# Kernel tuning notes

Measured on AMD Instinct MI355X. Metric: run time of the kernel, lower is better.

Reference implementation:

```python
import jax, jax.numpy as jnp
import numpy as np

N = 300000   # number of edges
MUL = 64     # multiplicity of each input irrep block
MID = 2 * MUL  # 128, simplified mid multiplicity per l


def setup_inputs() -> dict:
    key = jax.random.key(0)
    ks = jax.random.split(key, 12)
    inp = {
        # x: irreps 64x0e+64x1o -> [N, 64 + 64*3]
        "x": jax.random.normal(ks[0], (N, MUL + MUL * 3), dtype=jnp.float32),
        # y: irreps 1x0e+1x1o -> [N, 4] (edge spherical harmonics)
        "y": jax.random.normal(ks[1], (N, 4), dtype=jnp.float32),
        # scalars: 64x0e radial embedding
        "scalars": jax.random.normal(ks[2], (N, 64), dtype=jnp.float32),
        # uvw tensor-product weights, one [MUL, MUL] matrix per path (v dim = 1 squeezed)
        "W_tp1": jax.random.normal(ks[3], (MUL, MUL), dtype=jnp.float32),  # 0e x 0e -> 0e
        "W_tp2": jax.random.normal(ks[4], (MUL, MUL), dtype=jnp.float32),  # 0e x 1o -> 1o
        "W_tp3": jax.random.normal(ks[5], (MUL, MUL), dtype=jnp.float32),  # 1o x 0e -> 1o
        "W_tp4": jax.random.normal(ks[6], (MUL, MUL), dtype=jnp.float32),  # 1o x 1o -> 0e
        # radial MLP [64, 64, 64, 256]
        "W_fc1": jax.random.normal(ks[7], (64, 64), dtype=jnp.float32),
        "W_fc2": jax.random.normal(ks[8], (64, 64), dtype=jnp.float32),
        "W_fc3": jax.random.normal(ks[9], (64, 2 * MID), dtype=jnp.float32),
        # equivariant linear mix per l: 128 -> 64
        "W_lin0": jax.random.normal(ks[10], (MID, MUL), dtype=jnp.float32),
        "W_lin1": jax.random.normal(ks[11], (MID, MUL), dtype=jnp.float32),
    }
    return inp


def reference(x, y, scalars, W_tp1, W_tp2, W_tp3, W_tp4,
              W_fc1, W_fc2, W_fc3, W_lin0, W_lin1):
    n = x.shape[0]
    x0 = x[:, :MUL]                          # [N, 64]   0e
    x1 = x[:, MUL:].reshape(n, MUL, 3)       # [N, 64, 3] 1o
    y0 = y[:, 0:1]                           # [N, 1]    0e
    y1 = y[:, 1:4]                           # [N, 3]    1o

    inv_sqrt_mul = 1.0 / jnp.sqrt(jnp.float32(MUL))   # path normalization (fan_in = mul1*mul2)
    inv_sqrt3 = 1.0 / jnp.sqrt(jnp.float32(3.0))      # CG coeff for 1o x 1o -> 0e

    # --- uvw tensor product (4 paths), irreps_mid = 128x0e + 128x1o ---
    mid0a = ((x0 * y0) @ W_tp1) * inv_sqrt_mul                                 # [N,128? no: N,64] 0e
    mid0b = ((jnp.einsum('num,nm->nu', x1, y1) * inv_sqrt3) @ W_tp4) * inv_sqrt_mul  # [N,64] 0e
    mid1a = (x0 @ W_tp2)[:, :, None] * y1[:, None, :] * inv_sqrt_mul           # [N,64,3] 1o
    mid1b = jnp.einsum('num,uw->nwm', x1 * y0[:, :, None], W_tp3) * inv_sqrt_mul  # [N,64,3] 1o

    mid0 = jnp.concatenate([mid0a, mid0b], axis=1)   # [N,128]
    mid1 = jnp.concatenate([mid1a, mid1b], axis=1)   # [N,128,3]

    # --- radial MLP generating per-edge uvu scaling weights ---
    inv8 = 1.0 / jnp.sqrt(jnp.float32(64))
    h = jax.nn.silu((scalars @ W_fc1) * inv8)
    h = jax.nn.silu((h @ W_fc2) * inv8)
    w = (h @ W_fc3) * inv8                           # [N, 256]
    w0, w1 = w[:, :MID], w[:, MID:]

    # --- uvu scaling (tp of mid with 1x0e ones, per-edge weights) ---
    s0 = mid0 * w0                                   # [N,128]
    s1 = mid1 * w1[:, :, None]                       # [N,128,3]

    # --- o3.Linear 128x0e+128x1o -> 64x0e+64x1o ---
    inv_sqrt_mid = 1.0 / jnp.sqrt(jnp.float32(MID))
    out0 = (s0 @ W_lin0) * inv_sqrt_mid              # [N,64]
    out1 = jnp.einsum('num,uw->nwm', s1, W_lin1) * inv_sqrt_mid  # [N,64,3]

    return jnp.concatenate([out0, out1.reshape(n, MUL * 3)], axis=1)  # [N,256]
```

## Files before the change

### kernel.cpp

```cpp
#include <hip/hip_runtime.h>

typedef _Float16 f16x8 __attribute__((ext_vector_type(8)));
typedef float    f32x4 __attribute__((ext_vector_type(4)));

#define NROWS  300000
#define NTILES (NROWS/16)
#define WPB    8
#define TPB    512
#define NBLK   ((NTILES + WPB - 1) / WPB)

#define LSCALE     2048.0f
#define INV_LSCALE 4.8828125e-4f

#define RS64   136
#define LO64   72
#define RS128  264
#define LO128  136

#define IMG_P1 0
#define IMG_P2 17408
#define IMG_P3 34816
#define IMG_P4 52224
#define IMG_P5 78336
#define IMG_P6 95232
#define IMG_TOT 120832

#define BUFSZ  26112
#define OFF_A  0
#define OFF_B  BUFSZ
#define OFF_SBUF (2*BUFSZ)
#define SB_WAVE 1280
#define LDS_HALVES (OFF_SBUF + WPB*SB_WAVE)
static_assert(LDS_HALVES * 2 <= 160*1024, "LDS overflow");

struct fp16p { f16x8 h, l; };
struct h2 { _Float16 h, l; };
struct acc2 { f32x4 m, l; };

__device__ __forceinline__ f32x4 MFMA(f16x8 a, f16x8 b, f32x4 c) {
  return __builtin_amdgcn_mfma_f32_16x16x32_f16(a, b, c, 0, 0, 0);
}

__device__ __forceinline__ void gemm2(const fp16p& A0, const fp16p& B0,
                                      const fp16p& A1, const fp16p& B1, acc2& c) {
  c.m = MFMA(A0.h, B0.h, c.m);
  c.m = MFMA(A0.l, B0.h, c.m);
  c.l = MFMA(A0.h, B0.l, c.l);
  c.m = MFMA(A1.h, B1.h, c.m);
  c.m = MFMA(A1.l, B1.h, c.m);
  c.l = MFMA(A1.h, B1.l, c.l);
}
__device__ __forceinline__ f32x4 fin(const acc2& c) { return c.m + c.l * INV_LSCALE; }

__device__ __forceinline__ fp16p bfragp(const _Float16* w, int RS, int LO,
                                        int nt, int ks, int lane) {
  const _Float16* base = w + (nt*16 + (lane & 15))*RS + ks*32 + (lane >> 4)*8;
  fp16p r;
  r.h = *(const f16x8*)base;
  r.l = *(const f16x8*)(base + LO);
  return r;
}

__device__ __forceinline__ h2 split1(float v) {
  h2 r;
  r.h = (_Float16)v;
  r.l = (_Float16)(v - (float)r.h);
  return r;
}

__device__ __forceinline__ fp16p split8(const float* p, float s) {
  f32x4 a = *(const f32x4*)p, b = *(const f32x4*)(p + 4);
  fp16p r;
#pragma unroll
  for (int i = 0; i < 4; ++i) {
    h2 t0 = split1(a[i]*s);
    h2 t1 = split1(b[i]*s);
    r.h[i]   = t0.h; r.l[i]   = t0.l;
    r.h[4+i] = t1.h; r.l[4+i] = t1.l;
  }
  return r;
}

__device__ __forceinline__ void load24(const float* p, float* vv) {
#pragma unroll
  for (int i = 0; i < 6; ++i) {
    f32x4 t = *(const f32x4*)(p + 4*i);
    vv[4*i+0] = t[0]; vv[4*i+1] = t[1]; vv[4*i+2] = t[2]; vv[4*i+3] = t[3];
  }
}

__device__ __forceinline__ void copyimg(_Float16* ldsdst, const _Float16* gsrc,
                                        int nch, int wave, int lane) {
  for (int c = wave; c < nch; c += WPB)
    __builtin_amdgcn_global_load_lds(
        (const __attribute__((address_space(1))) void*)(gsrc + c*512 + lane*8),
        (__attribute__((address_space(3))) void*)(ldsdst + c*512), 16, 0, 0);
}

#define LGKM0() asm volatile("s_waitcnt lgkmcnt(0)" ::: "memory")

__global__ __launch_bounds__(256) void prep_w(
    const float* __restrict__ Wtp1, const float* __restrict__ Wtp2,
    const float* __restrict__ Wtp3, const float* __restrict__ Wtp4,
    const float* __restrict__ Wfc1, const float* __restrict__ Wfc2,
    const float* __restrict__ Wfc3, const float* __restrict__ Wlin0,
    const float* __restrict__ Wlin1, _Float16* __restrict__ ws)
{
  int e = blockIdx.x*256 + threadIdx.x;
  const float INV8 = 0.125f, INVS3 = 0.57735026918962576f, INVSMD = 0.08838834764831845f;
  const float* W; int u, n; _Float16* dst; int RS, LOo; float sc;
  if (e < 4096)       { int l = e;        u=l>>6; n=l&63;  W=Wfc1 +u*64+n;  dst=ws+IMG_P1;       RS=RS64;  LOo=LO64;  sc=INV8; }
  else if (e < 8192)  { int l = e-4096;   u=l>>6; n=l&63;  W=Wfc2 +u*64+n;  dst=ws+IMG_P1+8704;  RS=RS64;  LOo=LO64;  sc=INV8; }
  else if (e < 24576) { int l = e-8192;   u=l>>8; n=l&255; W=Wfc3 +u*256+n; RS=RS64; LOo=LO64; sc=INV8;
                        if (n < 128) dst = ws+IMG_P2; else { dst = ws+IMG_P3; n -= 128; } }
  else if (e < 28672) { int l = e-24576;  u=l>>6; n=l&63;  W=Wtp1 +u*64+n;  dst=ws+IMG_P4;       RS=RS64;  LOo=LO64;  sc=INV8; }
  else if (e < 32768) { int l = e-28672;  u=l>>6; n=l&63;  W=Wtp2 +u*64+n;  dst=ws+IMG_P4+8704;  RS=RS64;  LOo=LO64;  sc=INV8; }
  else if (e < 36864) { int l = e-32768;  u=l>>6; n=l&63;  W=Wtp4 +u*64+n;  dst=ws+IMG_P4+17408; RS=RS64;  LOo=LO64;  sc=INV8*INVS3; }
  else if (e < 45056) { int l = e-36864;  u=l>>6; n=l&63;  W=Wlin0+u*64+n;  dst=ws+IMG_P5;       RS=RS128; LOo=LO128; sc=INVSMD; }
  else if (e < 49152) { int l = e-45056;  u=l>>6; n=l&63;  W=Wtp3 +u*64+n;  dst=ws+IMG_P6;       RS=RS64;  LOo=LO64;  sc=INV8; }
  else                { int l = e-49152;  u=l>>6; n=l&63;  W=Wlin1+u*64+n;  dst=ws+IMG_P6+8704;  RS=RS128; LOo=LO128; sc=INVSMD; }
  float v = (*W) * sc;
  _Float16 h = (_Float16)v;
  float res = (v - (float)h) * LSCALE;
  dst[n*RS + u]       = h;
  dst[n*RS + LOo + u] = (_Float16)res;
}

__global__ __launch_bounds__(TPB, 2) void tp_fused(
    const float* __restrict__ x,    const float* __restrict__ y,
    const float* __restrict__ sc,
    const _Float16* __restrict__ wsrc, float* __restrict__ out)
{
  __shared__ _Float16 lds[LDS_HALVES];
  const int tid = threadIdx.x;
  const int lane = tid & 63;
  const int wave = tid >> 6;
  const int tile = blockIdx.x * WPB + wave;
  const bool active = (tile < NTILES);
  const int r0   = (active ? tile : 0) * 16;
  const int arow = lane & 15;
  const int kgrp = lane >> 4;
  const int rowg = r0 + arow;
  _Float16* bufA = lds + OFF_A;
  _Float16* bufB = lds + OFF_B;
  _Float16* swbh = lds + OFF_SBUF + wave*SB_WAVE;
  _Float16* swbl = swbh + 640;

  copyimg(bufA, wsrc + IMG_P1, 34, wave, lane);

  const float yv = y[r0*4 + lane];
  const float y0A  = __shfl(yv, arow*4 + 0);
  const float y1A0 = __shfl(yv, arow*4 + 1);
  const float y1A1 = __shfl(yv, arow*4 + 2);
  const float y1A2 = __shfl(yv, arow*4 + 3);
  float y1D[3][4];
#pragma unroll
  for (int m = 0; m < 3; ++m)
#pragma unroll
    for (int r = 0; r < 4; ++r)
      y1D[m][r] = __shfl(yv, (kgrp*4 + r)*4 + 1 + m);

  const int rbase = ((arow & 3)*4 + (arow >> 2))*40;
  auto bounce = [&](const f32x4* zz, bool do_silu, fp16p& A0, fp16p& A1) {
#pragma unroll
    for (int c = 0; c < 2; ++c) {
      LGKM0();
#pragma unroll
      for (int ntl = 0; ntl < 2; ++ntl)
#pragma unroll
        for (int r = 0; r < 4; ++r) {
          float v = zz[c*2 + ntl][r];
          if (do_silu) v = v / (1.f + __expf(-v));
          h2 t = split1(v);
          int o = (r*4 + kgrp)*40 + ntl*16 + arow;
          swbh[o] = t.h;
          swbl[o] = t.l;
        }
      LGKM0();
      fp16p& A = c ? A1 : A0;
      A.h = *(const f16x8*)(swbh + rbase + kgrp*8);
      A.l = *(const f16x8*)(swbl + rbase + kgrp*8);
    }
  };

  const float* scp = sc + rowg*64;
  fp16p A0 = split8(scp + kgrp*8, 1.f);
  fp16p A1 = split8(scp + 32 + kgrp*8, 1.f);

  __syncthreads();
  copyimg(bufB, wsrc + IMG_P2, 34, wave, lane);

  f32x4 z[4];
#pragma unroll
  for (int nt = 0; nt < 4; ++nt) {
    acc2 c{};
    gemm2(A0, bfragp(bufA, RS64, LO64, nt, 0, lane),
          A1, bfragp(bufA, RS64, LO64, nt, 1, lane), c);
    z[nt] = fin(c);
  }
  bounce(z, true, A0, A1);

  f32x4 z2[4];
#pragma unroll
  for (int nt = 0; nt < 4; ++nt) {
    acc2 c{};
    gemm2(A0, bfragp(bufA + 8704, RS64, LO64, nt, 0, lane),
          A1, bfragp(bufA + 8704, RS64, LO64, nt, 1, lane), c);
    z2[nt] = fin(c);
  }
  bounce(z2, true, A0, A1);

  __syncthreads();
  copyimg(bufA, wsrc + IMG_P3, 34, wave, lane);

  f32x4 w[16];
#pragma unroll
  for (int nt = 0; nt < 8; ++nt) {
    acc2 c{};
    gemm2(A0, bfragp(bufB, RS64, LO64, nt, 0, lane),
          A1, bfragp(bufB, RS64, LO64, nt, 1, lane), c);
    w[nt] = fin(c);
  }

  __syncthreads();
  copyimg(bufB, wsrc + IMG_P4, 51, wave, lane);

#pragma unroll
  for (int nt = 0; nt < 8; ++nt) {
    acc2 c{};
    gemm2(A0, bfragp(bufA, RS64, LO64, nt, 0, lane),
          A1, bfragp(bufA, RS64, LO64, nt, 1, lane), c);
    w[8 + nt] = fin(c);
  }

  __syncthreads();
  copyimg(bufA, wsrc + IMG_P5, 33, wave, lane);

  const float* xr = x + rowg*256;
  fp16p X0 = split8(xr + kgrp*8, 1.f);
  fp16p X1 = split8(xr + 32 + kgrp*8, 1.f);
  fp16p Aa0 = split8(xr + kgrp*8, y0A);
  fp16p Aa1 = split8(xr + 32 + kgrp*8, y0A);

  f32x4 t4[4];
  f32x4 m0[8];
#pragma unroll
  for (int nt = 0; nt < 4; ++nt) {
    acc2 ct{}, cm{};
    gemm2(X0,  bfragp(bufB + 8704, RS64, LO64, nt, 0, lane),
          X1,  bfragp(bufB + 8704, RS64, LO64, nt, 1, lane), ct);
    gemm2(Aa0, bfragp(bufB, RS64, LO64, nt, 0, lane),
          Aa1, bfragp(bufB, RS64, LO64, nt, 1, lane), cm);
    t4[nt] = fin(ct);
    m0[nt] = fin(cm);
  }

  fp16p B40, B41;
  {
    float vv[24];
    load24(xr + 64 + 3*(kgrp*8), vv);
#pragma unroll
    for (int j = 0; j < 8; ++j) {
      h2 t = split1(vv[3*j]*y1A0 + vv[3*j+1]*y1A1 + vv[3*j+2]*y1A2);
      B40.h[j] = t.h; B40.l[j] = t.l;
    }
    load24(xr + 64 + 3*(32 + kgrp*8), vv);
#pragma unroll
    for (int j = 0; j < 8; ++j) {
      h2 t = split1(vv[3*j]*y1A0 + vv[3*j+1]*y1A1 + vv[3*j+2]*y1A2);
      B41.h[j] = t.h; B41.l[j] = t.l;
    }
  }
#pragma unroll
  for (int nt = 0; nt < 4; ++nt) {
    acc2 c{};
    gemm2(B40, bfragp(bufB + 17408, RS64, LO64, nt, 0, lane),
          B41, bfragp(bufB + 17408, RS64, LO64, nt, 1, lane), c);
    m0[4+nt] = fin(c);
  }

  __syncthreads();
  copyimg(bufB, wsrc + IMG_P6, 50, wave, lane);

  acc2 o0c[4] = {};
#pragma unroll
  for (int half = 0; half < 2; ++half) {
    f32x4 s[4];
#pragma unroll
    for (int nt = 0; nt < 4; ++nt)
#pragma unroll
      for (int r = 0; r < 4; ++r)
        s[nt][r] = m0[half*4 + nt][r] * w[half*4 + nt][r];
    fp16p S0, S1;
    bounce(s, false, S0, S1);
#pragma unroll
    for (int nt = 0; nt < 4; ++nt)
      gemm2(S0, bfragp(bufA, RS128, LO128, nt, half*2+0, lane),
            S1, bfragp(bufA, RS128, LO128, nt, half*2+1, lane), o0c[nt]);
  }
  if (active) {
#pragma unroll
    for (int nt = 0; nt < 4; ++nt) {
      f32x4 v = fin(o0c[nt]);
#pragma unroll
      for (int r = 0; r < 4; ++r)
        out[(r0 + kgrp*4 + r)*256 + nt*16 + arow] = v[r];
    }
  }

  __syncthreads();

  f32x4 o1f[3][4];
#pragma unroll
  for (int m = 0; m < 3; ++m) {
    fp16p C0, C1;
    {
      float vv[24];
      load24(xr + 64 + 3*(kgrp*8), vv);
#pragma unroll
      for (int j = 0; j < 8; ++j) {
        h2 t = split1(vv[3*j + m] * y0A);
        C0.h[j] = t.h; C0.l[j] = t.l;
      }
      load24(xr + 64 + 3*(32 + kgrp*8), vv);
#pragma unroll
      for (int j = 0; j < 8; ++j) {
        h2 t = split1(vv[3*j + m] * y0A);
        C1.h[j] = t.h; C1.l[j] = t.l;
      }
    }
    f32x4 mb[4];
#pragma unroll
    for (int nt = 0; nt < 4; ++nt) {
      acc2 c{};
      gemm2(C0, bfragp(bufB, RS64, LO64, nt, 0, lane),
            C1, bfragp(bufB, RS64, LO64, nt, 1, lane), c);
      mb[nt] = fin(c);
    }

    acc2 o1c[4] = {};
    {
      f32x4 s[4];
#pragma unroll
      for (int nt = 0; nt < 4; ++nt)
#pragma unroll
        for (int r = 0; r < 4; ++r)
          s[nt][r] = t4[nt][r] * y1D[m][r] * w[8 + nt][r];
      fp16p S0, S1;
      bounce(s, false, S0, S1);
#pragma unroll
      for (int nt = 0; nt < 4; ++nt)
        gemm2(S0, bfragp(bufB + 8704, RS128, LO128, nt, 0, lane),
              S1, bfragp(bufB + 8704, RS128, LO128, nt, 1, lane), o1c[nt]);
    }
    {
      f32x4 s[4];
#pragma unroll
      for (int nt = 0; nt < 4; ++nt)
#pragma unroll
        for (int r = 0; r < 4; ++r)
          s[nt][r] = mb[nt][r] * w[12 + nt][r];
      fp16p S0, S1;
      bounce(s, false, S0, S1);
#pragma unroll
      for (int nt = 0; nt < 4; ++nt)
        gemm2(S0, bfragp(bufB + 8704, RS128, LO128, nt, 2, lane),
              S1, bfragp(bufB + 8704, RS128, LO128, nt, 3, lane), o1c[nt]);
    }
#pragma unroll
    for (int nt = 0; nt < 4; ++nt)
      o1f[m][nt] = fin(o1c[nt]);
  }

  if (active) {
#pragma unroll
    for (int nt = 0; nt < 4; ++nt)
#pragma unroll
      for (int r = 0; r < 4; ++r) {
        float* p = out + (r0 + kgrp*4 + r)*256 + 64 + (nt*16 + arow)*3;
        p[0] = o1f[0][nt][r];
        p[1] = o1f[1][nt][r];
        p[2] = o1f[2][nt][r];
      }
  }
}

extern "C" void kernel_launch(void* const* d_in, const int* in_sizes, int n_in,
                              void* d_out, int out_size, void* d_ws, size_t ws_size,
                              hipStream_t stream) {
  (void)in_sizes; (void)n_in; (void)out_size; (void)ws_size;
  _Float16* ws = (_Float16*)d_ws;
  prep_w<<<224, 256, 0, stream>>>(
      (const float*)d_in[3],  (const float*)d_in[4],  (const float*)d_in[5],
      (const float*)d_in[6],  (const float*)d_in[7],  (const float*)d_in[8],
      (const float*)d_in[9],  (const float*)d_in[10], (const float*)d_in[11], ws);
  tp_fused<<<NBLK, TPB, 0, stream>>>(
      (const float*)d_in[0],  (const float*)d_in[1],  (const float*)d_in[2],
      ws, (float*)d_out);
}
```

Measured before the change: 328.1 us.

## Use transposed 16x16x16 MFMA formulation to drop LDS bounce between layers

Reformulates every GEMM so weights act as the A operand and activations as the B operand, using the 16x16x16 f16 MFMA. In this form each layer's accumulator layout matches the next layer's input fragment layout, so the per-wave LDS bounce buffer, the shuffles and the lgkmcnt waits can be removed, and output rows are written as contiguous float4 stores. The trade-off is twice as many, smaller MFMA instructions and more LDS weight fragment loads of half width, with more registers held for the activation fragments.

```diff
diff --git a/kernel.cpp b/kernel.cpp
--- a/kernel.cpp
+++ b/kernel.cpp
@@ -1,6 +1,6 @@
 #include <hip/hip_runtime.h>
 
-typedef _Float16 f16x8 __attribute__((ext_vector_type(8)));
+typedef _Float16 f16x4 __attribute__((ext_vector_type(4)));
 typedef float    f32x4 __attribute__((ext_vector_type(4)));
 
 #define NROWS  300000
@@ -23,41 +23,35 @@
 #define IMG_P4 52224
 #define IMG_P5 78336
 #define IMG_P6 95232
-#define IMG_TOT 120832
 
 #define BUFSZ  26112
 #define OFF_A  0
 #define OFF_B  BUFSZ
-#define OFF_SBUF (2*BUFSZ)
-#define SB_WAVE 1280
-#define LDS_HALVES (OFF_SBUF + WPB*SB_WAVE)
+#define LDS_HALVES (2*BUFSZ)
 static_assert(LDS_HALVES * 2 <= 160*1024, "LDS overflow");
 
-struct fp16p { f16x8 h, l; };
-struct h2 { _Float16 h, l; };
-struct acc2 { f32x4 m, l; };
-
-__device__ __forceinline__ f32x4 MFMA(f16x8 a, f16x8 b, f32x4 c) {
-  return __builtin_amdgcn_mfma_f32_16x16x32_f16(a, b, c, 0, 0, 0);
-}
-
-__device__ __forceinline__ void gemm2(const fp16p& A0, const fp16p& B0,
-                                      const fp16p& A1, const fp16p& B1, acc2& c) {
-  c.m = MFMA(A0.h, B0.h, c.m);
-  c.m = MFMA(A0.l, B0.h, c.m);
-  c.l = MFMA(A0.h, B0.l, c.l);
-  c.m = MFMA(A1.h, B1.h, c.m);
-  c.m = MFMA(A1.l, B1.h, c.m);
-  c.l = MFMA(A1.h, B1.l, c.l);
+struct apair { f16x4 h, l; };
+struct bpair { f16x4 h, l; };
+struct h2    { _Float16 h, l; };
+struct acc2  { f32x4 m, l; };
+
+__device__ __forceinline__ f32x4 MFMA16(f16x4 a, f16x4 b, f32x4 c) {
+  return __builtin_amdgcn_mfma_f32_16x16x16f16(a, b, c, 0, 0, 0);
+}
+
+__device__ __forceinline__ void gemmT(const apair& a, const bpair& b, acc2& c) {
+  c.m = MFMA16(a.h, b.h, c.m);
+  c.m = MFMA16(a.h, b.l, c.m);
+  c.l = MFMA16(a.l, b.h, c.l);
 }
 __device__ __forceinline__ f32x4 fin(const acc2& c) { return c.m + c.l * INV_LSCALE; }
 
-__device__ __forceinline__ fp16p bfragp(const _Float16* w, int RS, int LO,
-                                        int nt, int ks, int lane) {
-  const _Float16* base = w + (nt*16 + (lane & 15))*RS + ks*32 + (lane >> 4)*8;
-  fp16p r;
-  r.h = *(const f16x8*)base;
-  r.l = *(const f16x8*)(base + LO);
+__device__ __forceinline__ apair afrag(const _Float16* w, int RS, int LO,
+                                       int nt, int ks, int lane) {
+  const _Float16* base = w + (nt*16 + (lane & 15))*RS + ks*16 + ((lane >> 4) << 2);
+  apair r;
+  r.h = *(const f16x4*)base;
+  r.l = *(const f16x4*)(base + LO);
   return r;
 }
 
@@ -68,25 +62,14 @@
   return r;
 }
 
-__device__ __forceinline__ fp16p split8(const float* p, float s) {
-  f32x4 a = *(const f32x4*)p, b = *(const f32x4*)(p + 4);
-  fp16p r;
+__device__ __forceinline__ bpair splitB(f32x4 v) {
+  bpair r;
 #pragma unroll
   for (int i = 0; i < 4; ++i) {
-    h2 t0 = split1(a[i]*s);
-    h2 t1 = split1(b[i]*s);
-    r.h[i]   = t0.h; r.l[i]   = t0.l;
-    r.h[4+i] = t1.h; r.l[4+i] = t1.l;
+    h2 t = split1(v[i]);
+    r.h[i] = t.h; r.l[i] = t.l;
   }
   return r;
-}
-
-__device__ __forceinline__ void load24(const float* p, float* vv) {
-#pragma unroll
-  for (int i = 0; i < 6; ++i) {
-    f32x4 t = *(const f32x4*)(p + 4*i);
-    vv[4*i+0] = t[0]; vv[4*i+1] = t[1]; vv[4*i+2] = t[2]; vv[4*i+3] = t[3];
-  }
 }
 
 __device__ __forceinline__ void copyimg(_Float16* ldsdst, const _Float16* gsrc,
@@ -96,8 +79,6 @@
         (const __attribute__((address_space(1))) void*)(gsrc + c*512 + lane*8),
         (__attribute__((address_space(3))) void*)(ldsdst + c*512), 16, 0, 0);
 }
-
-#define LGKM0() asm volatile("s_waitcnt lgkmcnt(0)" ::: "memory")
 
 __global__ __launch_bounds__(256) void prep_w(
     const float* __restrict__ Wtp1, const float* __restrict__ Wtp2,
@@ -132,7 +113,7 @@
     const _Float16* __restrict__ wsrc, float* __restrict__ out)
 {
   __shared__ _Float16 lds[LDS_HALVES];
-  const int tid = threadIdx.x;
+  const int tid  = threadIdx.x;
   const int lane = tid & 63;
   const int wave = tid >> 6;
   const int tile = blockIdx.x * WPB + wave;
@@ -143,241 +124,188 @@
   const int rowg = r0 + arow;
   _Float16* bufA = lds + OFF_A;
   _Float16* bufB = lds + OFF_B;
-  _Float16* swbh = lds + OFF_SBUF + wave*SB_WAVE;
-  _Float16* swbl = swbh + 640;
 
   copyimg(bufA, wsrc + IMG_P1, 34, wave, lane);
 
-  const float yv = y[r0*4 + lane];
-  const float y0A  = __shfl(yv, arow*4 + 0);
-  const float y1A0 = __shfl(yv, arow*4 + 1);
-  const float y1A1 = __shfl(yv, arow*4 + 2);
-  const float y1A2 = __shfl(yv, arow*4 + 3);
-  float y1D[3][4];
-#pragma unroll
-  for (int m = 0; m < 3; ++m)
-#pragma unroll
-    for (int r = 0; r < 4; ++r)
-      y1D[m][r] = __shfl(yv, (kgrp*4 + r)*4 + 1 + m);
-
-  const int rbase = ((arow & 3)*4 + (arow >> 2))*40;
-  auto bounce = [&](const f32x4* zz, bool do_silu, fp16p& A0, fp16p& A1) {
-#pragma unroll
-    for (int c = 0; c < 2; ++c) {
-      LGKM0();
-#pragma unroll
-      for (int ntl = 0; ntl < 2; ++ntl)
-#pragma unroll
-        for (int r = 0; r < 4; ++r) {
-          float v = zz[c*2 + ntl][r];
-          if (do_silu) v = v / (1.f + __expf(-v));
-          h2 t = split1(v);
-          int o = (r*4 + kgrp)*40 + ntl*16 + arow;
-          swbh[o] = t.h;
-          swbl[o] = t.l;
-        }
-      LGKM0();
-      fp16p& A = c ? A1 : A0;
-      A.h = *(const f16x8*)(swbh + rbase + kgrp*8);
-      A.l = *(const f16x8*)(swbl + rbase + kgrp*8);
+  f32x4 yr = *(const f32x4*)(y + rowg*4);
+  const float y0A = yr[0], y1A0 = yr[1], y1A1 = yr[2], y1A2 = yr[3];
+
+  const float* scp = sc + rowg*64;
+  bpair SC[4];
+#pragma unroll
+  for (int ks = 0; ks < 4; ++ks)
+    SC[ks] = splitB(*(const f32x4*)(scp + ks*16 + kgrp*4));
+
+  __syncthreads();
+  copyimg(bufB, wsrc + IMG_P2, 34, wave, lane);
+
+  bpair H[4];
+#pragma unroll
+  for (int nt = 0; nt < 4; ++nt) {
+    acc2 c{};
+#pragma unroll
+    for (int ks = 0; ks < 4; ++ks)
+      gemmT(afrag(bufA, RS64, LO64, nt, ks, lane), SC[ks], c);
+    f32x4 v = fin(c);
+#pragma unroll
+    for (int i = 0; i < 4; ++i) v[i] = v[i] / (1.f + __expf(-v[i]));
+    H[nt] = splitB(v);
+  }
+  bpair H2[4];
+#pragma unroll
+  for (int nt = 0; nt < 4; ++nt) {
+    acc2 c{};
+#pragma unroll
+    for (int ks = 0; ks < 4; ++ks)
+      gemmT(afrag(bufA + 8704, RS64, LO64, nt, ks, lane), H[ks], c);
+    f32x4 v = fin(c);
+#pragma unroll
+    for (int i = 0; i < 4; ++i) v[i] = v[i] / (1.f + __expf(-v[i]));
+    H2[nt] = splitB(v);
+  }
+
+  __syncthreads();
+  copyimg(bufA, wsrc + IMG_P3, 34, wave, lane);
+
+  f32x4 wv[16];
+#pragma unroll
+  for (int nt = 0; nt < 8; ++nt) {
+    acc2 c{};
+#pragma unroll
+    for (int ks = 0; ks < 4; ++ks)
+      gemmT(afrag(bufB, RS64, LO64, nt, ks, lane), H2[ks], c);
+    wv[nt] = fin(c);
+  }
+
+  __syncthreads();
+  copyimg(bufB, wsrc + IMG_P4, 51, wave, lane);
+
+#pragma unroll
+  for (int nt = 0; nt < 8; ++nt) {
+    acc2 c{};
+#pragma unroll
+    for (int ks = 0; ks < 4; ++ks)
+      gemmT(afrag(bufA, RS64, LO64, nt, ks, lane), H2[ks], c);
+    wv[8 + nt] = fin(c);
+  }
+
+  __syncthreads();
+  copyimg(bufA, wsrc + IMG_P5, 33, wave, lane);
+
+  const float* xr = x + rowg*256;
+  bpair X[4], Xa[4];
+#pragma unroll
+  for (int ks = 0; ks < 4; ++ks) {
+    f32x4 v = *(const f32x4*)(xr + ks*16 + kgrp*4);
+    X[ks]  = splitB(v);
+    Xa[ks] = splitB(v * y0A);
+  }
+
+  f32x4 t4T[4], m0T[8];
+#pragma unroll
+  for (int nt = 0; nt < 4; ++nt) {
+    acc2 ct{}, cm{};
+#pragma unroll
+    for (int ks = 0; ks < 4; ++ks) {
+      gemmT(afrag(bufB + 8704, RS64, LO64, nt, ks, lane), X[ks],  ct);
+      gemmT(afrag(bufB,        RS64, LO64, nt, ks, lane), Xa[ks], cm);
     }
-  };
-
-  const float* scp = sc + rowg*64;
-  fp16p A0 = split8(scp + kgrp*8, 1.f);
-  fp16p A1 = split8(scp + 32 + kgrp*8, 1.f);
-
-  __syncthreads();
-  copyimg(bufB, wsrc + IMG_P2, 34, wave, lane);
-
-  f32x4 z[4];
-#pragma unroll
-  for (int nt = 0; nt < 4; ++nt) {
-    acc2 c{};
-    gemm2(A0, bfragp(bufA, RS64, LO64, nt, 0, lane),
-          A1, bfragp(bufA, RS64, LO64, nt, 1, lane), c);
-    z[nt] = fin(c);
-  }
-  bounce(z, true, A0, A1);
-
-  f32x4 z2[4];
-#pragma unroll
-  for (int nt = 0; nt < 4; ++nt) {
-    acc2 c{};
-    gemm2(A0, bfragp(bufA + 8704, RS64, LO64, nt, 0, lane),
-          A1, bfragp(bufA + 8704, RS64, LO64, nt, 1, lane), c);
-    z2[nt] = fin(c);
-  }
-  bounce(z2, true, A0, A1);
-
-  __syncthreads();
-  copyimg(bufA, wsrc + IMG_P3, 34, wave, lane);
-
-  f32x4 w[16];
-#pragma unroll
-  for (int nt = 0; nt < 8; ++nt) {
-    acc2 c{};
-    gemm2(A0, bfragp(bufB, RS64, LO64, nt, 0, lane),
-          A1, bfragp(bufB, RS64, LO64, nt, 1, lane), c);
-    w[nt] = fin(c);
-  }
-
-  __syncthreads();
-  copyimg(bufB, wsrc + IMG_P4, 51, wave, lane);
-
-#pragma unroll
-  for (int nt = 0; nt < 8; ++nt) {
-    acc2 c{};
-    gemm2(A0, bfragp(bufA, RS64, LO64, nt, 0, lane),
-          A1, bfragp(bufA, RS64, LO64, nt, 1, lane), c);
-    w[8 + nt] = fin(c);
-  }
-
-  __syncthreads();
-  copyimg(bufA, wsrc + IMG_P5, 33, wave, lane);
-
-  const float* xr = x + rowg*256;
-  fp16p X0 = split8(xr + kgrp*8, 1.f);
-  fp16p X1 = split8(xr + 32 + kgrp*8, 1.f);
-  fp16p Aa0 = split8(xr + kgrp*8, y0A);
-  fp16p Aa1 = split8(xr + 32 + kgrp*8, y0A);
-
-  f32x4 t4[4];
-  f32x4 m0[8];
-#pragma unroll
-  for (int nt = 0; nt < 4; ++nt) {
-    acc2 ct{}, cm{};
-    gemm2(X0,  bfragp(bufB + 8704, RS64, LO64, nt, 0, lane),
-          X1,  bfragp(bufB + 8704, RS64, LO64, nt, 1, lane), ct);
-    gemm2(Aa0, bfragp(bufB, RS64, LO64, nt, 0, lane),
-          Aa1, bfragp(bufB, RS64, LO64, nt, 1, lane), cm);
-    t4[nt] = fin(ct);
-    m0[nt] = fin(cm);
-  }
-
-  fp16p B40, B41;
-  {
-    float vv[24];
-    load24(xr + 64 + 3*(kgrp*8), vv);
-#pragma unroll
-    for (int j = 0; j < 8; ++j) {
-      h2 t = split1(vv[3*j]*y1A0 + vv[3*j+1]*y1A1 + vv[3*j+2]*y1A2);
-      B40.h[j] = t.h; B40.l[j] = t.l;
+    t4T[nt] = fin(ct);
+    m0T[nt] = fin(cm);
+  }
+
+  bpair A1[4];
+#pragma unroll
+  for (int ks = 0; ks < 4; ++ks) {
+    const float* p = xr + 64 + (16*ks + 4*kgrp)*3;
+    f32x4 q0 = *(const f32x4*)p, q1 = *(const f32x4*)(p+4), q2 = *(const f32x4*)(p+8);
+    float vv[12];
+#pragma unroll
+    for (int i = 0; i < 4; ++i) { vv[i] = q0[i]; vv[4+i] = q1[i]; vv[8+i] = q2[i]; }
+    f32x4 a;
+#pragma unroll
+    for (int e = 0; e < 4; ++e)
+      a[e] = vv[3*e]*y1A0 + vv[3*e+1]*y1A1 + vv[3*e+2]*y1A2;
+    A1[ks] = splitB(a);
+  }
+#pragma unroll
+  for (int nt = 0; nt < 4; ++nt) {
+    acc2 c{};
+#pragma unroll
+    for (int ks = 0; ks < 4; ++ks)
+      gemmT(afrag(bufB + 17408, RS64, LO64, nt, ks, lane), A1[ks], c);
+    m0T[4 + nt] = fin(c);
+  }
+
+  __syncthreads();
+  copyimg(bufB, wsrc + IMG_P6, 50, wave, lane);
+
+  bpair S[8];
+#pragma unroll
+  for (int ks = 0; ks < 8; ++ks)
+    S[ks] = splitB(m0T[ks] * wv[ks]);
+#pragma unroll
+  for (int nt = 0; nt < 4; ++nt) {
+    acc2 c{};
+#pragma unroll
+    for (int ks = 0; ks < 8; ++ks)
+      gemmT(afrag(bufA, RS128, LO128, nt, ks, lane), S[ks], c);
+    if (active)
+      *(f32x4*)(out + (size_t)rowg*256 + nt*16 + kgrp*4) = fin(c);
+  }
+
+  __syncthreads();
+
+  f32x4 o1f[3][4];
+#pragma unroll
+  for (int m = 0; m < 3; ++m) {
+    const float y1m = (m == 0) ? y1A0 : (m == 1) ? y1A1 : y1A2;
+    bpair C[4];
+#pragma unroll
+    for (int ks = 0; ks < 4; ++ks) {
+      const float* p = xr + 64 + (16*ks + 4*kgrp)*3;
+      f32x4 q0 = *(const f32x4*)p, q1 = *(const f32x4*)(p+4), q2 = *(const f32x4*)(p+8);
+      float vv[12];
+#pragma unroll
+      for (int i = 0; i < 4; ++i) { vv[i] = q0[i]; vv[4+i] = q1[i]; vv[8+i] = q2[i]; }
+      f32x4 a;
+#pragma unroll
+      for (int e = 0; e < 4; ++e) a[e] = vv[3*e + m] * y0A;
+      C[ks] = splitB(a);
     }
-    load24(xr + 64 + 3*(32 + kgrp*8), vv);
-#pragma unroll
-    for (int j = 0; j < 8; ++j) {
-      h2 t = split1(vv[3*j]*y1A0 + vv[3*j+1]*y1A1 + vv[3*j+2]*y1A2);
-      B41.h[j] = t.h; B41.l[j] = t.l;
-    }
-  }
-#pragma unroll
-  for (int nt = 0; nt < 4; ++nt) {
-    acc2 c{};
-    gemm2(B40, bfragp(bufB + 17408, RS64, LO64, nt, 0, lane),
-          B41, bfragp(bufB + 17408, RS64, LO64, nt, 1, lane), c);
-    m0[4+nt] = fin(c);
-  }
-
-  __syncthreads();
-  copyimg(bufB, wsrc + IMG_P6, 50, wave, lane);
-
-  acc2 o0c[4] = {};
-#pragma unroll
-  for (int half = 0; half < 2; ++half) {
-    f32x4 s[4];
-#pragma unroll
-    for (int nt = 0; nt < 4; ++nt)
-#pragma unroll
-      for (int r = 0; r < 4; ++r)
-        s[nt][r] = m0[half*4 + nt][r] * w[half*4 + nt][r];
-    fp16p S0, S1;
-    bounce(s, false, S0, S1);
-#pragma unroll
-    for (int nt = 0; nt < 4; ++nt)
-      gemm2(S0, bfragp(bufA, RS128, LO128, nt, half*2+0, lane),
-            S1, bfragp(bufA, RS128, LO128, nt, half*2+1, lane), o0c[nt]);
-  }
-  if (active) {
-#pragma unroll
-    for (int nt = 0; nt < 4; ++nt) {
-      f32x4 v = fin(o0c[nt]);
-#pragma unroll
-      for (int r = 0; r < 4; ++r)
-        out[(r0 + kgrp*4 + r)*256 + nt*16 + arow] = v[r];
-    }
-  }
-
-  __syncthreads();
-
-  f32x4 o1f[3][4];
-#pragma unroll
-  for (int m = 0; m < 3; ++m) {
-    fp16p C0, C1;
-    {
-      float vv[24];
-      load24(xr + 64 + 3*(kgrp*8), vv);
-#pragma unroll
-      for (int j = 0; j < 8; ++j) {
-        h2 t = split1(vv[3*j + m] * y0A);
-        C0.h[j] = t.h; C0.l[j] = t.l;
-      }
-      load24(xr + 64 + 3*(32 + kgrp*8), vv);
-#pragma unroll
-      for (int j = 0; j < 8; ++j) {
-        h2 t = split1(vv[3*j + m] * y0A);
-        C1.h[j] = t.h; C1.l[j] = t.l;
-      }
-    }
-    f32x4 mb[4];
+    f32x4 mbT[4];
 #pragma unroll
     for (int nt = 0; nt < 4; ++nt) {
       acc2 c{};
-      gemm2(C0, bfragp(bufB, RS64, LO64, nt, 0, lane),
-            C1, bfragp(bufB, RS64, LO64, nt, 1, lane), c);
-      mb[nt] = fin(c);
+#pragma unroll
+      for (int ks = 0; ks < 4; ++ks)
+        gemmT(afrag(bufB, RS64, LO64, nt, ks, lane), C[ks], c);
+      mbT[nt] = fin(c);
     }
 
-    acc2 o1c[4] = {};
-    {
-      f32x4 s[4];
-#pragma unroll
-      for (int nt = 0; nt < 4; ++nt)
-#pragma unroll
-        for (int r = 0; r < 4; ++r)
-          s[nt][r] = t4[nt][r] * y1D[m][r] * w[8 + nt][r];
-      fp16p S0, S1;
-      bounce(s, false, S0, S1);
-#pragma unroll
-      for (int nt = 0; nt < 4; ++nt)
-        gemm2(S0, bfragp(bufB + 8704, RS128, LO128, nt, 0, lane),
-              S1, bfragp(bufB + 8704, RS128, LO128, nt, 1, lane), o1c[nt]);
+    bpair S1[8];
+#pragma unroll
+    for (int ks = 0; ks < 4; ++ks)
+      S1[ks] = splitB(t4T[ks] * y1m * wv[8 + ks]);
+#pragma unroll
+    for (int ks = 0; ks < 4; ++ks)
+      S1[4 + ks] = splitB(mbT[ks] * wv[12 + ks]);
+#pragma unroll
+    for (int nt = 0; nt < 4; ++nt) {
+      acc2 c{};
+#pragma unroll
+      for (int ks = 0; ks < 8; ++ks)
+        gemmT(afrag(bufB + 8704, RS128, LO128, nt, ks, lane), S1[ks], c);
+      o1f[m][nt] = fin(c);
     }
-    {
-      f32x4 s[4];
-#pragma unroll
-      for (int nt = 0; nt < 4; ++nt)
-#pragma unroll
-        for (int r = 0; r < 4; ++r)
-          s[nt][r] = mb[nt][r] * w[12 + nt][r];
-      fp16p S0, S1;
-      bounce(s, false, S0, S1);
-#pragma unroll
-      for (int nt = 0; nt < 4; ++nt)
-        gemm2(S0, bfragp(bufB + 8704, RS128, LO128, nt, 2, lane),
-              S1, bfragp(bufB + 8704, RS128, LO128, nt, 3, lane), o1c[nt]);
-    }
+  }
+
+  if (active) {
 #pragma unroll
     for (int nt = 0; nt < 4; ++nt)
-      o1f[m][nt] = fin(o1c[nt]);
-  }
-
-  if (active) {
-#pragma unroll
-    for (int nt = 0; nt < 4; ++nt)
 #pragma unroll
       for (int r = 0; r < 4; ++r) {
-        float* p = out + (r0 + kgrp*4 + r)*256 + 64 + (nt*16 + arow)*3;
+        float* p = out + (size_t)rowg*256 + 64 + (nt*16 + kgrp*4 + r)*3;
         p[0] = o1f[0][nt][r];
         p[1] = o1f[1][nt][r];
         p[2] = o1f[2][nt][r];
```

Measured after the change: 425.1 us. 1.3x slower.
